# Kernel tuning notes

Measured on AMD Instinct MI355X. Metric: run time of the kernel, lower is better.

## Reference

```python
import jax, jax.numpy as jnp
import numpy as np

D_STATE = 16
D_CONV = 4
EXPAND = 2
DT_RANK = 2  # ceil(d_model/16) for d_model=32
GROUPS = 4
EPS = 1e-5


def setup_inputs() -> dict:
    key = jax.random.key(0)
    ks = jax.random.split(key, 10)
    C = 32
    d_in = EXPAND * C  # 64
    B, H, W = 2, 256, 256
    s = 0.02
    x = jax.random.normal(ks[0], (B, C, H, W), jnp.float32)
    W_in = jax.random.normal(ks[1], (C, 2 * d_in), jnp.float32) * s
    conv_w = jax.random.normal(ks[2], (d_in, D_CONV), jnp.float32) * 0.3
    conv_b = jnp.zeros((d_in,), jnp.float32)
    W_xproj = jax.random.normal(ks[3], (d_in, DT_RANK + 2 * D_STATE), jnp.float32) * s
    W_dt = jax.random.normal(ks[4], (DT_RANK, d_in), jnp.float32) * (DT_RANK ** -0.5)
    b_dt = jnp.full((d_in,), -3.0, jnp.float32)  # softplus(-3) ~ 0.05 dt init
    A_log = jnp.log(jnp.tile(jnp.arange(1.0, D_STATE + 1.0, dtype=jnp.float32), (d_in, 1)))
    Dp = jnp.ones((d_in,), jnp.float32)
    W_out = jax.random.normal(ks[5], (d_in, C), jnp.float32) * s
    gn_gamma = jnp.ones((C,), jnp.float32)
    gn_beta = jnp.zeros((C,), jnp.float32)
    return {"x": x, "W_in": W_in, "conv_w": conv_w, "conv_b": conv_b,
            "W_xproj": W_xproj, "W_dt": W_dt, "b_dt": b_dt, "A_log": A_log,
            "Dp": Dp, "W_out": W_out, "gn_gamma": gn_gamma, "gn_beta": gn_beta}


def reference(x, W_in, conv_w, conv_b, W_xproj, W_dt, b_dt, A_log, Dp, W_out, gn_gamma, gn_beta):
    B, C, H, W = x.shape
    d_in = W_in.shape[1] // 2
    L = B * H * W
    # [B,C,H,W] -> [B,H,W,C] -> [L,C] (batch folded into sequence, as in source)
    xf = jnp.transpose(x, (0, 2, 3, 1)).reshape(L, C)
    xz = xf @ W_in                       # [L, 2*d_in]
    u, z = xz[:, :d_in], xz[:, d_in:]
    # causal depthwise conv1d, kernel D_CONV, padding D_CONV-1, truncated to L
    up = jnp.pad(u, ((D_CONV - 1, 0), (0, 0)))
    uc = conv_b
    for k in range(D_CONV):
        uc = uc + up[k:k + L] * conv_w[:, k]
    uc = uc * jax.nn.sigmoid(uc)         # SiLU
    dbc = uc @ W_xproj                   # [L, dt_rank + 2*d_state]
    dt = dbc[:, :DT_RANK]
    Bm = dbc[:, DT_RANK:DT_RANK + D_STATE]   # [L, d_state]
    Cm = dbc[:, DT_RANK + D_STATE:]          # [L, d_state]
    delta = jax.nn.softplus(dt @ W_dt + b_dt)  # [L, d_in]
    A = -jnp.exp(A_log)                  # [d_in, d_state]

    def step(h, inp):
        d_t, B_t, C_t, u_t = inp
        h = jnp.exp(d_t[:, None] * A) * h + (d_t * u_t)[:, None] * B_t[None, :]
        return h, (h * C_t[None, :]).sum(-1)

    h0 = jnp.zeros((d_in, D_STATE), xf.dtype)
    _, ys = jax.lax.scan(step, h0, (delta, Bm, Cm, uc))  # ys: [L, d_in]
    y = ys + Dp * uc
    y = y * (z * jax.nn.sigmoid(z))      # gate with SiLU(z)
    out = (y @ W_out).reshape(B, H, W, C).transpose(0, 3, 1, 2)  # [B,C,H,W]
    # GroupNorm(4, C) + SiLU
    g = out.reshape(B, GROUPS, C // GROUPS, H, W)
    mu = g.mean((2, 3, 4), keepdims=True)
    var = g.var((2, 3, 4), keepdims=True)
    g = (g - mu) * jax.lax.rsqrt(var + EPS)
    out = g.reshape(B, C, H, W) * gn_gamma[None, :, None, None] + gn_beta[None, :, None, None]
    out = out * jax.nn.sigmoid(out)
    return out + x
```

## Files before the change

### kernel.cpp

```cpp
#include <hip/hip_runtime.h>

#define L_TOT   131072
#define HW      65536
#define CCH     32
#define DIN     64
#define NCHUNK  4096
#define TCH     32
#define NGRP    128
#define GCH     32
#define NBLK    (L_TOT/64)


typedef short bf16x8 __attribute__((ext_vector_type(8)));
typedef float f32x4  __attribute__((ext_vector_type(4)));

__device__ __forceinline__ float sigmoidf_(float x){ return 1.0f/(1.0f + __expf(-x)); }

__device__ __forceinline__ unsigned short f2bf(float f){
    union { float f; unsigned int u; } v; v.f = f;
    unsigned int u = v.u;
    return (unsigned short)((u + 0x7fffu + ((u >> 16) & 1u)) >> 16);
}
__device__ __forceinline__ float bf2f(unsigned short s){
    union { unsigned int u; float f; } v; v.u = ((unsigned int)s) << 16;
    return v.f;
}

__global__ void __launch_bounds__(256)
k_halo(const float* __restrict__ x, const float* __restrict__ W_in,
       float* __restrict__ u_halo){
    int tid = blockIdx.x*256 + threadIdx.x;
    int j  = tid & 63;
    int bh = tid >> 6;
    int b  = bh / 3;
    int hi = bh - b*3;
    float acc = 0.f;
    if (b > 0){
        int token = b*64 - 3 + hi;
        const float* xp = x + ((size_t)(token >> 16))*CCH*HW + (size_t)(token & (HW-1));
        #pragma unroll
        for (int c=0;c<CCH;c++)
            acc = fmaf(xp[(size_t)c*HW], W_in[c*2*DIN + j], acc);
    }
    u_halo[tid] = acc;
}

#define OFF_US   0
#define OFF_WIN  4556
#define OFF_OUT  7116
#define OFF_WXT  9420
#define LDS_FLOATS 11148

__global__ void __launch_bounds__(256)
k_front(const float* __restrict__ x, const float* __restrict__ W_in,
        const float* __restrict__ conv_w, const float* __restrict__ conv_b,
        const float* __restrict__ W_xproj, const float* __restrict__ W_dt,
        const float* __restrict__ b_dt, const float* __restrict__ u_halo,
        float* __restrict__ z, float* __restrict__ uc,
        float* __restrict__ delta, float* __restrict__ Bm, float* __restrict__ Cm,
        float* __restrict__ S, float* __restrict__ sd){
    __shared__ float lds[LDS_FLOATS];
    unsigned short* Wb = (unsigned short*)(lds + OFF_WIN);
    unsigned short* Xb = (unsigned short*)(lds + OFF_OUT);
    unsigned short* Wx = (unsigned short*)(lds + OFF_WXT);
    unsigned short* Ub = (unsigned short*)(lds + OFF_WIN);
    const int tid  = threadIdx.x;
    const int w    = tid >> 6;
    const int lane = tid & 63;
    const int base = blockIdx.x * 64;

    #pragma unroll
    for (int it=0; it<16; it++){
        int c = it*2 + (tid>>7);
        int j = tid & 127;
        Wb[j*40 + c] = f2bf(W_in[c*128 + j]);
    }
    {
        int c  = tid >> 3;
        int t8 = (tid & 7) * 8;
        const float* xp = x + (size_t)(base >> 16)*CCH*HW + (base & (HW-1)) + (size_t)c*HW + t8;
        float4 v0 = ((const float4*)xp)[0];
        float4 v1 = ((const float4*)xp)[1];
        float xs[8] = {v0.x,v0.y,v0.z,v0.w, v1.x,v1.y,v1.z,v1.w};
        #pragma unroll
        for (int i=0;i<8;i++) Xb[(t8+i)*40 + c] = f2bf(xs[i]);
    }
    #pragma unroll
    for (int it=0; it<9; it++){
        int f = it*256 + tid;
        if (f < 2176){
            int dd = f / 34;
            int mm = f - dd*34;
            Wx[mm*72 + dd] = f2bf(W_xproj[f]);
        }
    }
    {
        unsigned int* Wxu = (unsigned int*)Wx;
        if (tid < 252){ Wxu[1224 + tid] = 0u; Wxu[1224 + 252 + tid] = 0u; }
    }
    if (tid < 192)
        lds[OFF_US + (tid>>6)*68 + (tid&63)] = u_halo[blockIdx.x*192 + tid];
    __syncthreads();

    {
        const int j0w = w*32;
        bf16x8 af[4];
        #pragma unroll
        for (int tt=0; tt<4; tt++)
            af[tt] = *reinterpret_cast<const bf16x8*>(&Xb[(tt*16 + (lane&15))*40 + (lane>>4)*8]);
        f32x4 acc[4][2];
        #pragma unroll
        for (int tt=0; tt<4; tt++){ acc[tt][0]=(f32x4)0.f; acc[tt][1]=(f32x4)0.f; }
        #pragma unroll
        for (int jt=0; jt<2; jt++){
            bf16x8 bfr = *reinterpret_cast<const bf16x8*>(&Wb[(j0w + jt*16 + (lane&15))*40 + (lane>>4)*8]);
            #pragma unroll
            for (int tt=0; tt<4; tt++)
                acc[tt][jt] = __builtin_amdgcn_mfma_f32_16x16x32_bf16(af[tt], bfr, acc[tt][jt], 0, 0, 0);
        }
        if (w < 2){
            #pragma unroll
            for (int tt=0; tt<4; tt++)
                #pragma unroll
                for (int jt=0; jt<2; jt++){
                    int j = j0w + jt*16 + (lane&15);
                    #pragma unroll
                    for (int r=0;r<4;r++){
                        int t = tt*16 + (lane>>4)*4 + r;
                        lds[OFF_US + (t+3)*68 + j] = acc[tt][jt][r];
                    }
                }
        } else {
            #pragma unroll
            for (int tt=0; tt<4; tt++)
                #pragma unroll
                for (int jt=0; jt<2; jt++){
                    int j = j0w - 64 + jt*16 + (lane&15);
                    #pragma unroll
                    for (int r=0;r<4;r++){
                        int t = tt*16 + (lane>>4)*4 + r;
                        z[(size_t)(base+t)*DIN + j] = acc[tt][jt][r];
                    }
                }
        }
    }
    __syncthreads();

    {
        int d = lane;
        float4 cwv = reinterpret_cast<const float4*>(conv_w)[d];
        float  cb  = conv_b[d];
        #pragma unroll
        for (int i=0;i<16;i++){
            int tl = w*16 + i;
            float v = cb;
            v = fmaf(lds[OFF_US + (tl+0)*68 + d], cwv.x, v);
            v = fmaf(lds[OFF_US + (tl+1)*68 + d], cwv.y, v);
            v = fmaf(lds[OFF_US + (tl+2)*68 + d], cwv.z, v);
            v = fmaf(lds[OFF_US + (tl+3)*68 + d], cwv.w, v);
            v = v * sigmoidf_(v);
            unsigned short us = f2bf(v);
            uc[(size_t)(base + tl)*DIN + d] = bf2f(us);
            Ub[tl*72 + d] = us;
        }
    }
    __syncthreads();

    {
        f32x4 acc3[3];
        acc3[0]=(f32x4)0.f; acc3[1]=(f32x4)0.f; acc3[2]=(f32x4)0.f;
        #pragma unroll
        for (int k=0; k<2; k++){
            bf16x8 au = *reinterpret_cast<const bf16x8*>(&Ub[(w*16 + (lane&15))*72 + k*32 + (lane>>4)*8]);
            #pragma unroll
            for (int mt=0; mt<3; mt++){
                bf16x8 bw = *reinterpret_cast<const bf16x8*>(&Wx[(mt*16 + (lane&15))*72 + k*32 + (lane>>4)*8]);
                acc3[mt] = __builtin_amdgcn_mfma_f32_16x16x32_bf16(au, bw, acc3[mt], 0, 0, 0);
            }
        }
        __syncthreads();
        #pragma unroll
        for (int mt=0; mt<3; mt++){
            int m = mt*16 + (lane&15);
            if (m < 34){
                int col = (m < 2) ? m : m + 2;
                #pragma unroll
                for (int r=0;r<4;r++){
                    int t = w*16 + (lane>>4)*4 + r;
                    lds[OFF_OUT + t*36 + col] = acc3[mt][r];
                }
            }
        }
    }
    __syncthreads();

    {
        int dd = lane;
        float wdt0 = W_dt[dd], wdt1 = W_dt[DIN+dd], bdd = b_dt[dd];
        #pragma unroll
        for (int it=0; it<16; it++){
            int t = it*4 + w;
            float dt0 = lds[OFF_OUT + t*36 + 0];
            float dt1 = lds[OFF_OUT + t*36 + 1];
            float pre = fmaf(dt0, wdt0, fmaf(dt1, wdt1, bdd));
            float v = (pre > 20.f) ? pre : __logf(1.f + __expf(pre));
            delta[(size_t)(base + t)*DIN + dd] = v;
            lds[OFF_US + t*68 + dd] = v;
        }
        {
            int t = tid >> 2, q = tid & 3;
            float4 vb = *reinterpret_cast<const float4*>(&lds[OFF_OUT + t*36 + 4  + q*4]);
            float4 vc = *reinterpret_cast<const float4*>(&lds[OFF_OUT + t*36 + 20 + q*4]);
            *reinterpret_cast<float4*>(Bm + (size_t)(base+t)*16 + q*4) = vb;
            *reinterpret_cast<float4*>(Cm + (size_t)(base+t)*16 + q*4) = vc;
        }
    }
    __syncthreads();

    {
        int c  = tid >> 7;
        int hh = (tid >> 6) & 1;
        int d  = tid & 63;
        float h8[8];
        #pragma unroll
        for (int k=0;k<8;k++) h8[k]=0.f;
        float sdl = 0.f;
        #pragma unroll 4
        for (int tt=0; tt<TCH; tt++){
            int tl = c*32 + tt;
            float dl = lds[OFF_US + tl*68 + d];
            float uu = bf2f(Ub[tl*72 + d]);
            float4 bq0 = *reinterpret_cast<const float4*>(&lds[OFF_OUT + tl*36 + 4 + hh*8]);
            float4 bq1 = *reinterpret_cast<const float4*>(&lds[OFF_OUT + tl*36 + 8 + hh*8]);
            float bbv[8] = {bq0.x,bq0.y,bq0.z,bq0.w, bq1.x,bq1.y,bq1.z,bq1.w};
            float e1 = __expf(-dl);
            float e2 = e1*e1, e4 = e2*e2, e8 = e4*e4;
            float aa = hh ? (e8*e1) : e1;
            float du = dl*uu;
            sdl += dl;
            #pragma unroll
            for (int k=0;k<8;k++){
                h8[k] = fmaf(aa, h8[k], du*bbv[k]);
                aa *= e1;
            }
        }
        int chunk = blockIdx.x*2 + c;
        float4* So = (float4*)(S + (size_t)chunk*1024 + d*16 + hh*8);
        So[0] = make_float4(h8[0],h8[1],h8[2],h8[3]);
        So[1] = make_float4(h8[4],h8[5],h8[6],h8[7]);
        if (hh == 0) sd[chunk*64 + d] = sdl;
    }
}

__global__ void k_scan2a(float* __restrict__ S, float* __restrict__ sd,
                         float* __restrict__ Sg, float* __restrict__ sdg){
    int gt = blockIdx.x*blockDim.x + threadIdx.x;
    int g  = gt >> 10;
    int e  = gt & 1023;
    int d  = e >> 4;
    float f = (float)((e & 15) + 1);
    float ps = 0.f, s = 0.f;
    for (int i=0;i<GCH;i++){
        int chunk = g*GCH + i;
        size_t idx = (size_t)chunk*1024 + e;
        float sc  = S[idx];
        float sdc = sd[chunk*64 + d];
        S[idx] = s;
        if ((e & 15) == 0) sd[chunk*64 + d] = ps;
        float pc = __expf(-sdc * f);
        s = fmaf(s, pc, sc);
        ps += sdc;
    }
    Sg[g*1024 + e] = s;
    if ((e & 15) == 0) sdg[g*64 + d] = ps;
}

__global__ void k_scan2b(const float* __restrict__ Sg, const float* __restrict__ sdg,
                         float* __restrict__ Hg){
    int e = threadIdx.x;
    int d = e >> 4;
    float f = (float)((e & 15) + 1);
    float h = 0.f;
    for (int g=0; g<NGRP; g++){
        Hg[g*1024 + e] = h;
        float pg = __expf(-sdg[g*64 + d] * f);
        h = fmaf(pg, h, Sg[g*1024 + e]);
    }
}

__global__ void __launch_bounds__(256)
k_back(const float* __restrict__ delta, const float* __restrict__ uc,
       const float* __restrict__ Bm, const float* __restrict__ Cm,
       const float* __restrict__ z,
       const float* __restrict__ S, const float* __restrict__ sd,
       const float* __restrict__ Hg, const float* __restrict__ Dp,
       const float* __restrict__ W_out,
       float* __restrict__ o, float* __restrict__ stats){
    __shared__ float ys[128*68];
    __shared__ float red[2][8];
    int tid  = threadIdx.x;
    int wid  = tid >> 6;
    int d    = tid & 63;
    int chunk = blockIdx.x*4 + wid;
    int g = chunk >> 5;

    float h[16];
    {
        size_t sbase = (size_t)chunk*1024 + d*16;
        float psdl = sd[chunk*64 + d];
        const float* Hr = Hg + (size_t)g*1024 + d*16;
        #pragma unroll
        for (int n=0;n<16;n++){
            float pex = __expf(-psdl * (float)(n+1));
            h[n] = fmaf(pex, Hr[n], S[sbase + n]);
        }
    }
    float Dpd = Dp[d];
    int t0 = chunk*TCH;
    const float* dp = delta + (size_t)t0*DIN + d;
    const float* up = uc    + (size_t)t0*DIN + d;
    const float* zp = z     + (size_t)t0*DIN + d;
    const float4* B4 = (const float4*)(Bm + (size_t)t0*16);
    const float4* C4 = (const float4*)(Cm + (size_t)t0*16);

    float  ndl = dp[0], nuu = up[0], nzz = zp[0];
    float4 nb0=B4[0], nb1=B4[1], nb2=B4[2], nb3=B4[3];
    float4 nc0=C4[0], nc1=C4[1], nc2=C4[2], nc3=C4[3];

    for (int tt=0; tt<TCH; tt++){
        float dl=ndl, uu=nuu, zz=nzz;
        float4 b0=nb0,b1=nb1,b2=nb2,b3=nb3;
        float4 c0=nc0,c1=nc1,c2=nc2,c3=nc3;
        if (tt+1 < TCH){
            ndl = dp[(size_t)(tt+1)*DIN]; nuu = up[(size_t)(tt+1)*DIN]; nzz = zp[(size_t)(tt+1)*DIN];
            nb0 = B4[(tt+1)*4+0]; nb1 = B4[(tt+1)*4+1]; nb2 = B4[(tt+1)*4+2]; nb3 = B4[(tt+1)*4+3];
            nc0 = C4[(tt+1)*4+0]; nc1 = C4[(tt+1)*4+1]; nc2 = C4[(tt+1)*4+2]; nc3 = C4[(tt+1)*4+3];
        }
        float bb[16] = {b0.x,b0.y,b0.z,b0.w, b1.x,b1.y,b1.z,b1.w,
                        b2.x,b2.y,b2.z,b2.w, b3.x,b3.y,b3.z,b3.w};
        float cc[16] = {c0.x,c0.y,c0.z,c0.w, c1.x,c1.y,c1.z,c1.w,
                        c2.x,c2.y,c2.z,c2.w, c3.x,c3.y,c3.z,c3.w};
        float e1 = __expf(-dl);
        float e2 = e1*e1;
        float a[16];
        a[0]=e1; a[1]=e2;
        #pragma unroll
        for (int n=2;n<16;n++) a[n] = a[n-2]*e2;
        float du = dl*uu;
        float yv = 0.f;
        #pragma unroll
        for (int n=0;n<16;n++){
            h[n] = fmaf(a[n], h[n], du*bb[n]);
            yv   = fmaf(h[n], cc[n], yv);
        }
        yv = fmaf(Dpd, uu, yv);
        yv *= zz * sigmoidf_(zz);
        ys[(wid*32 + tt)*68 + d] = yv;
    }
    __syncthreads();

    if (tid < 128){
        int tl = tid;
        int t  = blockIdx.x*128 + tl;
        float acc[CCH];
        #pragma unroll
        for (int j=0;j<CCH;j++) acc[j]=0.f;
        #pragma unroll
        for (int q=0;q<DIN/4;q++){
            const float4 v = *reinterpret_cast<const float4*>(&ys[tl*68 + q*4]);
            float vv[4] = {v.x, v.y, v.z, v.w};
            #pragma unroll
            for (int r=0;r<4;r++){
                int dd = 4*q+r;
                float yd = vv[r];
                #pragma unroll
                for (int j=0;j<CCH;j++) acc[j] = fmaf(yd, W_out[dd*CCH+j], acc[j]);
            }
        }
        float4* o4 = (float4*)(o + (size_t)t*CCH);
        #pragma unroll
        for (int q=0;q<CCH/4;q++) o4[q] = make_float4(acc[4*q],acc[4*q+1],acc[4*q+2],acc[4*q+3]);

        int wv = tl >> 6;
        #pragma unroll
        for (int gg=0; gg<4; gg++){
            float s = 0.f, q2 = 0.f;
            #pragma unroll
            for (int r=0;r<8;r++){ float v = acc[gg*8+r]; s += v; q2 = fmaf(v,v,q2); }
            #pragma unroll
            for (int off=32; off>0; off>>=1){
                s  += __shfl_down(s,  off);
                q2 += __shfl_down(q2, off);
            }
            if ((tl & 63) == 0){ red[wv][gg*2] = s; red[wv][gg*2+1] = q2; }
        }
    }
    __syncthreads();
    if (tid < 8){
        int b = (blockIdx.x*128) >> 16;
        float s = red[0][tid] + red[1][tid];
        atomicAdd(&stats[b*8 + tid], s);
    }
}

__global__ void k_final(const float* __restrict__ o, const float* __restrict__ x,
                        const float* __restrict__ stats, const float* __restrict__ gn_gamma,
                        const float* __restrict__ gn_beta, float* __restrict__ out){
    int t  = blockIdx.x*blockDim.x + threadIdx.x;
    int b  = t >> 16;
    int hw = t & (HW-1);
    float mu[4], rs[4];
    #pragma unroll
    for (int gg=0; gg<4; gg++){
        float sm = stats[b*8+gg*2], sq = stats[b*8+gg*2+1];
        const float invN = 1.f/524288.f;
        float m = sm*invN;
        float var = fmaf(sq, invN, -m*m);
        mu[gg]=m; rs[gg]=rsqrtf(var + 1e-5f);
    }
    const float4* o4 = (const float4*)(o + (size_t)t*CCH);
    const float* xb = x + (size_t)b*CCH*HW + hw;
    float* ob = out + (size_t)b*CCH*HW + hw;
    #pragma unroll
    for (int q=0;q<CCH/4;q++){
        float4 v = o4[q];
        float vv[4] = {v.x, v.y, v.z, v.w};
        #pragma unroll
        for (int r=0;r<4;r++){
            int j = 4*q+r;
            int gg = j >> 3;
            float val = fmaf((vv[r]-mu[gg])*rs[gg], gn_gamma[j], gn_beta[j]);
            val = val * sigmoidf_(val);
            ob[(size_t)j*HW] = val + xb[(size_t)j*HW];
        }
    }
}

extern "C" void kernel_launch(void* const* d_in, const int* in_sizes, int n_in,
                              void* d_out, int out_size, void* d_ws, size_t ws_size,
                              hipStream_t stream) {
    const float* x       = (const float*)d_in[0];
    const float* W_in    = (const float*)d_in[1];
    const float* conv_w  = (const float*)d_in[2];
    const float* conv_b  = (const float*)d_in[3];
    const float* W_xproj = (const float*)d_in[4];
    const float* W_dt    = (const float*)d_in[5];
    const float* b_dt    = (const float*)d_in[6];
    const float* Dp      = (const float*)d_in[8];
    const float* W_out   = (const float*)d_in[9];
    const float* gn_gamma= (const float*)d_in[10];
    const float* gn_beta = (const float*)d_in[11];
    float* out = (float*)d_out;

    const size_t N_LD = (size_t)L_TOT * DIN;
    float* w     = (float*)d_ws;
    float* z     = w;
    float* uc    = z + N_LD;
    float* delta = uc + N_LD;
    float* Bm    = delta + N_LD;
    float* Cm    = Bm + (size_t)L_TOT*16;
    float* S     = Cm + (size_t)L_TOT*16;
    float* sd    = S  + (size_t)NCHUNK*1024;
    float* Sg    = sd + (size_t)NCHUNK*64;
    float* sdg   = Sg + (size_t)NGRP*1024;
    float* Hg    = sdg+ (size_t)NGRP*64;
    float* stats = Hg + (size_t)NGRP*1024;
    float* o     = stats + 16;
    float* u_halo= o + (size_t)L_TOT*CCH;

    hipMemsetAsync(stats, 0, 16*sizeof(float), stream);

    k_halo  <<<(NBLK*3*64)/256, 256, 0, stream>>>(x, W_in, u_halo);
    k_front <<<NBLK, 256, 0, stream>>>(x, W_in, conv_w, conv_b, W_xproj, W_dt, b_dt,
                                       u_halo, z, uc, delta, Bm, Cm, S, sd);
    k_scan2a<<<(NGRP*1024)/256, 256, 0, stream>>>(S, sd, Sg, sdg);
    k_scan2b<<<1, 1024, 0, stream>>>(Sg, sdg, Hg);
    k_back  <<<NCHUNK/4, 256, 0, stream>>>(delta, uc, Bm, Cm, z, S, sd, Hg, Dp, W_out,
                                           o, stats);
    k_final <<<L_TOT/256, 256, 0, stream>>>(o, x, stats, gn_gamma, gn_beta, out);
}
```

Measured before the change: 156.8 us.

## Split scan state across two threads per channel in back kernel

```diff
diff --git a/kernel.cpp b/kernel.cpp
--- a/kernel.cpp
+++ b/kernel.cpp
@@ -296,23 +296,28 @@
        const float* __restrict__ Hg, const float* __restrict__ Dp,
        const float* __restrict__ W_out,
        float* __restrict__ o, float* __restrict__ stats){
-    __shared__ float ys[128*68];
-    __shared__ float red[2][8];
-    int tid  = threadIdx.x;
-    int wid  = tid >> 6;
-    int d    = tid & 63;
-    int chunk = blockIdx.x*4 + wid;
+    __shared__ float ys[64*68];
+    int tid = threadIdx.x;
+    int c   = tid >> 7;
+    int d   = (tid >> 1) & 63;
+    int hh  = tid & 1;
+    int chunk = blockIdx.x*2 + c;
     int g = chunk >> 5;
 
-    float h[16];
-    {
-        size_t sbase = (size_t)chunk*1024 + d*16;
+    float h8[8];
+    {
         float psdl = sd[chunk*64 + d];
-        const float* Hr = Hg + (size_t)g*1024 + d*16;
-        #pragma unroll
-        for (int n=0;n<16;n++){
-            float pex = __expf(-psdl * (float)(n+1));
-            h[n] = fmaf(pex, Hr[n], S[sbase + n]);
+        const float4* Sr = (const float4*)(S  + (size_t)chunk*1024 + d*16 + hh*8);
+        const float4* Hr = (const float4*)(Hg + (size_t)g*1024     + d*16 + hh*8);
+        float4 s0 = Sr[0], s1 = Sr[1];
+        float4 h0 = Hr[0], h1 = Hr[1];
+        float sv[8] = {s0.x,s0.y,s0.z,s0.w, s1.x,s1.y,s1.z,s1.w};
+        float hv[8] = {h0.x,h0.y,h0.z,h0.w, h1.x,h1.y,h1.z,h1.w};
+        #pragma unroll
+        for (int k=0;k<8;k++){
+            float n1 = (float)(hh*8 + k + 1);
+            float pex = __expf(-psdl * n1);
+            h8[k] = fmaf(pex, hv[k], sv[k]);
         }
     }
     float Dpd = Dp[d];
@@ -320,48 +325,44 @@
     const float* dp = delta + (size_t)t0*DIN + d;
     const float* up = uc    + (size_t)t0*DIN + d;
     const float* zp = z     + (size_t)t0*DIN + d;
-    const float4* B4 = (const float4*)(Bm + (size_t)t0*16);
-    const float4* C4 = (const float4*)(Cm + (size_t)t0*16);
+    const float4* B4 = (const float4*)(Bm + (size_t)t0*16) + hh*2;
+    const float4* C4 = (const float4*)(Cm + (size_t)t0*16) + hh*2;
 
     float  ndl = dp[0], nuu = up[0], nzz = zp[0];
-    float4 nb0=B4[0], nb1=B4[1], nb2=B4[2], nb3=B4[3];
-    float4 nc0=C4[0], nc1=C4[1], nc2=C4[2], nc3=C4[3];
+    float4 nb0 = B4[0], nb1 = B4[1];
+    float4 nc0 = C4[0], nc1 = C4[1];
 
     for (int tt=0; tt<TCH; tt++){
         float dl=ndl, uu=nuu, zz=nzz;
-        float4 b0=nb0,b1=nb1,b2=nb2,b3=nb3;
-        float4 c0=nc0,c1=nc1,c2=nc2,c3=nc3;
+        float4 b0=nb0, b1=nb1, c0=nc0, c1=nc1;
         if (tt+1 < TCH){
             ndl = dp[(size_t)(tt+1)*DIN]; nuu = up[(size_t)(tt+1)*DIN]; nzz = zp[(size_t)(tt+1)*DIN];
-            nb0 = B4[(tt+1)*4+0]; nb1 = B4[(tt+1)*4+1]; nb2 = B4[(tt+1)*4+2]; nb3 = B4[(tt+1)*4+3];
-            nc0 = C4[(tt+1)*4+0]; nc1 = C4[(tt+1)*4+1]; nc2 = C4[(tt+1)*4+2]; nc3 = C4[(tt+1)*4+3];
-        }
-        float bb[16] = {b0.x,b0.y,b0.z,b0.w, b1.x,b1.y,b1.z,b1.w,
-                        b2.x,b2.y,b2.z,b2.w, b3.x,b3.y,b3.z,b3.w};
-        float cc[16] = {c0.x,c0.y,c0.z,c0.w, c1.x,c1.y,c1.z,c1.w,
-                        c2.x,c2.y,c2.z,c2.w, c3.x,c3.y,c3.z,c3.w};
+            nb0 = B4[(tt+1)*4+0]; nb1 = B4[(tt+1)*4+1];
+            nc0 = C4[(tt+1)*4+0]; nc1 = C4[(tt+1)*4+1];
+        }
+        float bbv[8] = {b0.x,b0.y,b0.z,b0.w, b1.x,b1.y,b1.z,b1.w};
+        float ccv[8] = {c0.x,c0.y,c0.z,c0.w, c1.x,c1.y,c1.z,c1.w};
         float e1 = __expf(-dl);
-        float e2 = e1*e1;
-        float a[16];
-        a[0]=e1; a[1]=e2;
-        #pragma unroll
-        for (int n=2;n<16;n++) a[n] = a[n-2]*e2;
+        float e2 = e1*e1, e4 = e2*e2, e8 = e4*e4;
+        float aa = hh ? (e8*e1) : e1;
         float du = dl*uu;
         float yv = 0.f;
         #pragma unroll
-        for (int n=0;n<16;n++){
-            h[n] = fmaf(a[n], h[n], du*bb[n]);
-            yv   = fmaf(h[n], cc[n], yv);
-        }
+        for (int k=0;k<8;k++){
+            h8[k] = fmaf(aa, h8[k], du*bbv[k]);
+            yv    = fmaf(h8[k], ccv[k], yv);
+            aa   *= e1;
+        }
+        yv += __shfl_xor(yv, 1);
         yv = fmaf(Dpd, uu, yv);
         yv *= zz * sigmoidf_(zz);
-        ys[(wid*32 + tt)*68 + d] = yv;
-    }
-    __syncthreads();
-
-    if (tid < 128){
+        if (hh == 0) ys[(c*32 + tt)*68 + d] = yv;
+    }
+    __syncthreads();
+
+    if (tid < 64){
         int tl = tid;
-        int t  = blockIdx.x*128 + tl;
+        int t  = blockIdx.x*64 + tl;
         float acc[CCH];
         #pragma unroll
         for (int j=0;j<CCH;j++) acc[j]=0.f;
@@ -381,7 +382,7 @@
         #pragma unroll
         for (int q=0;q<CCH/4;q++) o4[q] = make_float4(acc[4*q],acc[4*q+1],acc[4*q+2],acc[4*q+3]);
 
-        int wv = tl >> 6;
+        int b = (blockIdx.x*64) >> 16;
         #pragma unroll
         for (int gg=0; gg<4; gg++){
             float s = 0.f, q2 = 0.f;
@@ -392,14 +393,11 @@
                 s  += __shfl_down(s,  off);
                 q2 += __shfl_down(q2, off);
             }
-            if ((tl & 63) == 0){ red[wv][gg*2] = s; red[wv][gg*2+1] = q2; }
-        }
-    }
-    __syncthreads();
-    if (tid < 8){
-        int b = (blockIdx.x*128) >> 16;
-        float s = red[0][tid] + red[1][tid];
-        atomicAdd(&stats[b*8 + tid], s);
+            if (tid == 0){
+                atomicAdd(&stats[b*8 + gg*2 + 0], s);
+                atomicAdd(&stats[b*8 + gg*2 + 1], q2);
+            }
+        }
     }
 }
 
@@ -475,7 +473,7 @@
                                        u_halo, z, uc, delta, Bm, Cm, S, sd);
     k_scan2a<<<(NGRP*1024)/256, 256, 0, stream>>>(S, sd, Sg, sdg);
     k_scan2b<<<1, 1024, 0, stream>>>(Sg, sdg, Hg);
-    k_back  <<<NCHUNK/4, 256, 0, stream>>>(delta, uc, Bm, Cm, z, S, sd, Hg, Dp, W_out,
+    k_back  <<<NCHUNK/2, 256, 0, stream>>>(delta, uc, Bm, Cm, z, S, sd, Hg, Dp, W_out,
                                            o, stats);
     k_final <<<L_TOT/256, 256, 0, stream>>>(o, x, stats, gn_gamma, gn_beta, out);
 }
```

New measurement: 343.4 us. 2.19x slower.
